# Kernel tuning notes

Measured on AMD Instinct MI355X. Metric: run time of the kernel, lower is better.

The kernel has to match this reference:

```python
import jax, jax.numpy as jnp
import numpy as np

G = 64        # groups (experts)
T = 8192      # num_tokens
DIN = 2560    # in_features
DOUT = 1664   # out_features
CAP = 2 * (T // G)  # static per-expert capacity (= 256), bounds every group size


def setup_inputs() -> dict:
    key = jax.random.key(0)
    k1, k2, k3, k4 = jax.random.split(key, 4)
    x = jax.random.normal(k1, (T, DIN), dtype=jnp.float32)
    w = jax.random.normal(k2, (G, DIN, DOUT), dtype=jnp.float32) * 0.02
    # ragged group sizes: mean T//G = 128, each in [0, 256], summing exactly to T
    base = T // G
    r = jax.random.randint(k3, (G // 2,), 0, base + 1)
    delta = jax.random.permutation(k4, jnp.concatenate([r, -r]))
    counts = (base + delta).astype(jnp.int32)
    return {"input": x, "weight": w, "tokens_per_expert": counts}


def _grouped_gemm(x, w, counts):
    # tokens are laid out contiguously by expert: group g owns rows
    # [starts[g], starts[g]+counts[g])
    starts = jnp.concatenate([jnp.zeros((1,), counts.dtype), jnp.cumsum(counts)[:-1]])
    ids = jnp.repeat(jnp.arange(G, dtype=counts.dtype), counts, total_repeat_length=T)  # [T] expert id per token
    pos = jnp.arange(T, dtype=counts.dtype) - starts[ids]   # position within its group
    dest = ids * CAP + pos                                   # slot in padded [G*CAP] buffer
    # scatter tokens into a fixed-capacity padded buffer, one batched GEMM, gather back
    buf = jnp.zeros((G * CAP, DIN), x.dtype).at[dest].set(x)
    y = jnp.einsum('gci,gio->gco', buf.reshape(G, CAP, DIN), w)  # [G, CAP, DOUT]
    return y.reshape(G * CAP, DOUT)[dest]                        # [T, DOUT]


def reference(input, weight, tokens_per_expert):
    return _grouped_gemm(input, weight, tokens_per_expert)
```

## Files before the change

kernel.cpp:

```cpp
#include <hip/hip_runtime.h>
#include <stdint.h>

#define NG   64
#define NTOK 8192
#define KDIM 2560
#define NDIM 1664
#define BM   128
#define BN   128
#define BK   32
#define NKITER (KDIM / BK)
#define ASTRIDE 40

typedef __attribute__((ext_vector_type(8))) short bf16x8;
typedef __attribute__((ext_vector_type(4))) float f32x4;
typedef __attribute__((ext_vector_type(4))) unsigned int u32x4;
typedef __attribute__((ext_vector_type(2))) unsigned int u32x2;

static __device__ __forceinline__ unsigned pk2(float a, float b) {
    unsigned ua = __float_as_uint(a) + 0x8000u;
    unsigned ub = __float_as_uint(b) + 0x8000u;
    return __builtin_amdgcn_perm(ub, ua, 0x07060302u);
}

__global__ __launch_bounds__(256, 2)
void grouped_gemm(const float* __restrict__ X, const float* __restrict__ W,
                  const int* __restrict__ counts, float* __restrict__ Y) {
    const int nt = blockIdx.x;
    const int mt = blockIdx.y;
    const int g  = blockIdx.z;

    int start = 0, cnt = 0;
    #pragma unroll 1
    for (int i = 0; i < NG; ++i) {
        int c = counts[i];
        start += (i < g) ? c : 0;
        cnt = (i == g) ? c : cnt;
    }
    const int m0 = mt * BM;
    if (m0 >= cnt) return;
    const int nb = nt * BN;

    const int tid  = threadIdx.x;
    const int lane = tid & 63;
    const int wid  = tid >> 6;
    const int wm   = (wid >> 1) * 64;
    const int wn   = (wid & 1) * 64;

    __shared__ unsigned short Ash[BM * ASTRIDE];
    __shared__ unsigned short Bsh[BN * BK];

    const int ar  = tid >> 2;
    const int akq = (tid & 3) * 8;
    int gr0 = start + m0 + ar;       if (gr0 > NTOK - 1) gr0 = NTOK - 1;
    int gr1 = start + m0 + ar + 64;  if (gr1 > NTOK - 1) gr1 = NTOK - 1;
    const float* ap0 = X + (size_t)gr0 * KDIM + akq;
    const float* ap1 = X + (size_t)gr1 * KDIM + akq;

    const int l5  = tid & 31;
    const int bk4 = (tid >> 5) * 4;
    const int bn0 = l5 * 4;
    const float* bp = W + (size_t)g * KDIM * NDIM + (size_t)bk4 * NDIM + nb + bn0;
    const int bw0 = bn0 * BK + ((bk4 >> 3) ^ (l5 & 3)) * 8 + ((bk4 >> 2) & 1) * 4;

    f32x4 acc[4][4];
    #pragma unroll
    for (int i = 0; i < 4; ++i)
        #pragma unroll
        for (int j = 0; j < 4; ++j)
            acc[i][j] = (f32x4)0.0f;

    const int fm = lane & 15;
    const int fq = lane >> 4;

    f32x4 a0 = *(const f32x4*)(ap0);        f32x4 a1 = *(const f32x4*)(ap0 + 4);
    f32x4 a2 = *(const f32x4*)(ap1);        f32x4 a3 = *(const f32x4*)(ap1 + 4);
    f32x4 b0 = *(const f32x4*)(bp);
    f32x4 b1 = *(const f32x4*)(bp + NDIM);
    f32x4 b2 = *(const f32x4*)(bp + 2 * NDIM);
    f32x4 b3 = *(const f32x4*)(bp + 3 * NDIM);
    ap0 += BK; ap1 += BK; bp += (size_t)BK * NDIM;

    for (int kt = 0; kt < NKITER; ++kt) {
        __syncthreads();
        u32x4 pa0 = { pk2(a0[0],a0[1]), pk2(a0[2],a0[3]), pk2(a1[0],a1[1]), pk2(a1[2],a1[3]) };
        u32x4 pa1 = { pk2(a2[0],a2[1]), pk2(a2[2],a2[3]), pk2(a3[0],a3[1]), pk2(a3[2],a3[3]) };
        *(u32x4*)&Ash[ar * ASTRIDE + akq]        = pa0;
        *(u32x4*)&Ash[(ar + 64) * ASTRIDE + akq] = pa1;
        #pragma unroll
        for (int j = 0; j < 4; ++j) {
            u32x2 pb = { pk2(b0[j], b1[j]), pk2(b2[j], b3[j]) };
            *(u32x2*)&Bsh[bw0 + j * BK] = pb;
        }
        __syncthreads();
        if (kt + 1 < NKITER) {
            a0 = *(const f32x4*)(ap0);      a1 = *(const f32x4*)(ap0 + 4);
            a2 = *(const f32x4*)(ap1);      a3 = *(const f32x4*)(ap1 + 4);
            b0 = *(const f32x4*)(bp);
            b1 = *(const f32x4*)(bp + NDIM);
            b2 = *(const f32x4*)(bp + 2 * NDIM);
            b3 = *(const f32x4*)(bp + 3 * NDIM);
            ap0 += BK; ap1 += BK; bp += (size_t)BK * NDIM;
        }
        bf16x8 af[4], bfr[4];
        #pragma unroll
        for (int i = 0; i < 4; ++i)
            af[i] = *(const bf16x8*)&Ash[(wm + i * 16 + fm) * ASTRIDE + fq * 8];
        #pragma unroll
        for (int j = 0; j < 4; ++j) {
            int n  = wn + j * 16 + fm;
            int su = fq ^ ((n >> 2) & 3);
            bfr[j] = *(const bf16x8*)&Bsh[n * BK + su * 8];
        }
        #pragma unroll
        for (int i = 0; i < 4; ++i)
            #pragma unroll
            for (int j = 0; j < 4; ++j)
                acc[i][j] = __builtin_amdgcn_mfma_f32_16x16x32_bf16(af[i], bfr[j], acc[i][j], 0, 0, 0);
    }

    const int r4 = fq * 4;
    #pragma unroll
    for (int i = 0; i < 4; ++i) {
        int mlbase = m0 + wm + i * 16 + r4;
        #pragma unroll
        for (int j = 0; j < 4; ++j) {
            int col = nb + wn + j * 16 + fm;
            #pragma unroll
            for (int rr = 0; rr < 4; ++rr) {
                int row = mlbase + rr;
                if (row < cnt)
                    Y[(size_t)(start + row) * NDIM + col] = acc[i][j][rr];
            }
        }
    }
}

extern "C" void kernel_launch(void* const* d_in, const int* in_sizes, int n_in,
                              void* d_out, int out_size, void* d_ws, size_t ws_size,
                              hipStream_t stream) {
    const float* X      = (const float*)d_in[0];
    const float* W      = (const float*)d_in[1];
    const int*   counts = (const int*)d_in[2];
    float*       Y      = (float*)d_out;
    dim3 grid(NDIM / BN, 2, NG);
    grouped_gemm<<<grid, 256, 0, stream>>>(X, W, counts, Y);
}
```

Baseline: 1.584 ms.

## Double-buffer LDS tiles, wave-scan expert offsets, and reshape weight loads

Replaces the serial 64-iteration prefix loop over counts with a wavefront shuffle scan. Shared A/B tiles are double-buffered, which removes the leading barrier in each K iteration. The weight tile is now loaded as 8 rows of float2 per thread and written to LDS as 16-byte packed stores, with a new swizzle. Launch bounds request 3 blocks per CU. The extra LDS and register pressure at the higher occupancy target could cause spills or limit residency.

Result: no change. 1.604 ms (+1.3%).

```diff
diff --git a/kernel.cpp b/kernel.cpp
--- a/kernel.cpp
+++ b/kernel.cpp
@@ -9,12 +9,12 @@
 #define BN   128
 #define BK   32
 #define NKITER (KDIM / BK)
-#define ASTRIDE 40
+#define ASTR 40
 
 typedef __attribute__((ext_vector_type(8))) short bf16x8;
 typedef __attribute__((ext_vector_type(4))) float f32x4;
+typedef __attribute__((ext_vector_type(2))) float f32x2;
 typedef __attribute__((ext_vector_type(4))) unsigned int u32x4;
-typedef __attribute__((ext_vector_type(2))) unsigned int u32x2;
 
 static __device__ __forceinline__ unsigned pk2(float a, float b) {
     unsigned ua = __float_as_uint(a) + 0x8000u;
@@ -22,32 +22,36 @@
     return __builtin_amdgcn_perm(ub, ua, 0x07060302u);
 }
 
-__global__ __launch_bounds__(256, 2)
+__global__ __launch_bounds__(256, 3)
 void grouped_gemm(const float* __restrict__ X, const float* __restrict__ W,
                   const int* __restrict__ counts, float* __restrict__ Y) {
     const int nt = blockIdx.x;
     const int mt = blockIdx.y;
     const int g  = blockIdx.z;
 
-    int start = 0, cnt = 0;
-    #pragma unroll 1
-    for (int i = 0; i < NG; ++i) {
-        int c = counts[i];
-        start += (i < g) ? c : 0;
-        cnt = (i == g) ? c : cnt;
+    const int tid  = threadIdx.x;
+    const int lane = tid & 63;
+    const int wid  = tid >> 6;
+
+    int c    = counts[lane];
+    int incl = c;
+    #pragma unroll
+    for (int off = 1; off < 64; off <<= 1) {
+        int y = __shfl_up(incl, off, 64);
+        if (lane >= off) incl += y;
     }
+    const int cnt   = __shfl(c, g, 64);
+    const int start = __shfl(incl, g, 64) - cnt;
+
     const int m0 = mt * BM;
     if (m0 >= cnt) return;
     const int nb = nt * BN;
 
-    const int tid  = threadIdx.x;
-    const int lane = tid & 63;
-    const int wid  = tid >> 6;
-    const int wm   = (wid >> 1) * 64;
-    const int wn   = (wid & 1) * 64;
+    const int wm = (wid >> 1) * 64;
+    const int wn = (wid & 1) * 64;
 
-    __shared__ unsigned short Ash[BM * ASTRIDE];
-    __shared__ unsigned short Bsh[BN * BK];
+    __shared__ unsigned short Ash[2][BM * ASTR];
+    __shared__ unsigned short Bsh[2][BN * BK];
 
     const int ar  = tid >> 2;
     const int akq = (tid & 3) * 8;
@@ -56,11 +60,8 @@
     const float* ap0 = X + (size_t)gr0 * KDIM + akq;
     const float* ap1 = X + (size_t)gr1 * KDIM + akq;
 
-    const int l5  = tid & 31;
-    const int bk4 = (tid >> 5) * 4;
-    const int bn0 = l5 * 4;
-    const float* bp = W + (size_t)g * KDIM * NDIM + (size_t)bk4 * NDIM + nb + bn0;
-    const int bw0 = bn0 * BK + ((bk4 >> 3) ^ (l5 & 3)) * 8 + ((bk4 >> 2) & 1) * 4;
+    const float* bp = W + (size_t)g * KDIM * NDIM + (size_t)(wid * 8) * NDIM + nb + lane * 2;
+    const int bw0 = (lane * 2) * BK + ((wid ^ (lane & 3)) * 8);
 
     f32x4 acc[4][4];
     #pragma unroll
@@ -72,44 +73,42 @@
     const int fm = lane & 15;
     const int fq = lane >> 4;
 
-    f32x4 a0 = *(const f32x4*)(ap0);        f32x4 a1 = *(const f32x4*)(ap0 + 4);
-    f32x4 a2 = *(const f32x4*)(ap1);        f32x4 a3 = *(const f32x4*)(ap1 + 4);
-    f32x4 b0 = *(const f32x4*)(bp);
-    f32x4 b1 = *(const f32x4*)(bp + NDIM);
-    f32x4 b2 = *(const f32x4*)(bp + 2 * NDIM);
-    f32x4 b3 = *(const f32x4*)(bp + 3 * NDIM);
+    f32x4 a0 = *(const f32x4*)(ap0);  f32x4 a1 = *(const f32x4*)(ap0 + 4);
+    f32x4 a2 = *(const f32x4*)(ap1);  f32x4 a3 = *(const f32x4*)(ap1 + 4);
+    f32x2 wv[8];
+    #pragma unroll
+    for (int r = 0; r < 8; ++r) wv[r] = *(const f32x2*)(bp + (size_t)r * NDIM);
     ap0 += BK; ap1 += BK; bp += (size_t)BK * NDIM;
 
     for (int kt = 0; kt < NKITER; ++kt) {
-        __syncthreads();
+        const int b = kt & 1;
         u32x4 pa0 = { pk2(a0[0],a0[1]), pk2(a0[2],a0[3]), pk2(a1[0],a1[1]), pk2(a1[2],a1[3]) };
         u32x4 pa1 = { pk2(a2[0],a2[1]), pk2(a2[2],a2[3]), pk2(a3[0],a3[1]), pk2(a3[2],a3[3]) };
-        *(u32x4*)&Ash[ar * ASTRIDE + akq]        = pa0;
-        *(u32x4*)&Ash[(ar + 64) * ASTRIDE + akq] = pa1;
+        *(u32x4*)&Ash[b][ar * ASTR + akq]        = pa0;
+        *(u32x4*)&Ash[b][(ar + 64) * ASTR + akq] = pa1;
         #pragma unroll
-        for (int j = 0; j < 4; ++j) {
-            u32x2 pb = { pk2(b0[j], b1[j]), pk2(b2[j], b3[j]) };
-            *(u32x2*)&Bsh[bw0 + j * BK] = pb;
+        for (int jj = 0; jj < 2; ++jj) {
+            u32x4 pb = { pk2(wv[0][jj], wv[1][jj]), pk2(wv[2][jj], wv[3][jj]),
+                         pk2(wv[4][jj], wv[5][jj]), pk2(wv[6][jj], wv[7][jj]) };
+            *(u32x4*)&Bsh[b][bw0 + jj * BK] = pb;
         }
         __syncthreads();
         if (kt + 1 < NKITER) {
-            a0 = *(const f32x4*)(ap0);      a1 = *(const f32x4*)(ap0 + 4);
-            a2 = *(const f32x4*)(ap1);      a3 = *(const f32x4*)(ap1 + 4);
-            b0 = *(const f32x4*)(bp);
-            b1 = *(const f32x4*)(bp + NDIM);
-            b2 = *(const f32x4*)(bp + 2 * NDIM);
-            b3 = *(const f32x4*)(bp + 3 * NDIM);
+            a0 = *(const f32x4*)(ap0);  a1 = *(const f32x4*)(ap0 + 4);
+            a2 = *(const f32x4*)(ap1);  a3 = *(const f32x4*)(ap1 + 4);
+            #pragma unroll
+            for (int r = 0; r < 8; ++r) wv[r] = *(const f32x2*)(bp + (size_t)r * NDIM);
             ap0 += BK; ap1 += BK; bp += (size_t)BK * NDIM;
         }
         bf16x8 af[4], bfr[4];
         #pragma unroll
         for (int i = 0; i < 4; ++i)
-            af[i] = *(const bf16x8*)&Ash[(wm + i * 16 + fm) * ASTRIDE + fq * 8];
+            af[i] = *(const bf16x8*)&Ash[b][(wm + i * 16 + fm) * ASTR + fq * 8];
         #pragma unroll
         for (int j = 0; j < 4; ++j) {
             int n  = wn + j * 16 + fm;
-            int su = fq ^ ((n >> 2) & 3);
-            bfr[j] = *(const bf16x8*)&Bsh[n * BK + su * 8];
+            int su = fq ^ ((n >> 1) & 3);
+            bfr[j] = *(const bf16x8*)&Bsh[b][n * BK + su * 8];
         }
         #pragma unroll
         for (int i = 0; i < 4; ++i)
```
